# Kernel tuning notes

Measured on AMD Instinct MI355X. Metric: run time of the kernel, lower is better.

Reference implementation:

```python
import jax, jax.numpy as jnp
import numpy as np

ATTN_RNN_DIM, EMB_DIM, ATTN_DIM = 1024, 512, 128
N_FILT, KSIZE = 32, 31
B, T = 64, 2048


def setup_inputs() -> dict:
    key = jax.random.key(0)
    ks = jax.random.split(key, 8)
    return {
        "attention_rnn_h": jax.random.normal(ks[0], (B, ATTN_RNN_DIM), jnp.float32),
        "memory": jax.random.normal(ks[1], (B, T, EMB_DIM), jnp.float32),
        "processed_memory": jax.random.normal(ks[2], (B, T, ATTN_DIM), jnp.float32),
        "attention_weights_cat": jax.random.uniform(ks[3], (B, 2, T), jnp.float32),
        "memory_mask": jnp.zeros((B, T), jnp.bool_),
        # learned params
        "W_query": jax.random.normal(ks[4], (ATTN_DIM, ATTN_RNN_DIM), jnp.float32) * 0.02,
        "conv_w": jax.random.normal(ks[5], (N_FILT, 2, KSIZE), jnp.float32) * 0.05,
        "W_dense": jax.random.normal(ks[6], (ATTN_DIM, N_FILT), jnp.float32) * 0.05,
        "w_v": jax.random.normal(ks[7], (1, ATTN_DIM), jnp.float32) * 0.05,
    }


def reference(attention_rnn_h, memory, processed_memory, attention_weights_cat,
              memory_mask, W_query, conv_w, W_dense, w_v):
    pad = (KSIZE - 1) // 2
    # location conv: (B,2,T) -> (B,N_FILT,T), no bias, 'same' padding
    loc = jax.lax.conv_general_dilated(
        attention_weights_cat, conv_w, window_strides=(1,),
        padding=[(pad, pad)], dimension_numbers=("NCH", "OIH", "NCH"))
    # location dense: (B,T,N_FILT) @ W_dense.T -> (B,T,ATTN_DIM)
    processed_loc = jnp.einsum("bft,df->btd", loc, W_dense)
    # processed query: (B,1,ATTN_DIM)
    processed_query = (attention_rnn_h @ W_query.T)[:, None, :]
    # additive energy: w^T tanh(q + loc + mem) -> (B,T)
    energy = jnp.tanh(processed_query + processed_loc + processed_memory)
    alignment = jnp.einsum("btd,d->bt", energy, w_v[0])
    alignment = jnp.where(memory_mask, -jnp.inf, alignment)
    attention_weights = jax.nn.softmax(alignment, axis=1)  # over T
    # context: (B,1,T) @ (B,T,E) -> (B,E)
    attention_context = jnp.einsum("bt,bte->be", attention_weights, memory)
    return attention_context, attention_weights
```

## Files before the change

kernel.cpp:

```cpp
#include <hip/hip_runtime.h>
#include <math.h>

#define B_SZ 64
#define T_SZ 2048
#define EMB 512
#define ADIM 128
#define NFILT 32
#define KSZ 31
#define TT 64

__device__ __forceinline__ float fast_tanh(float x) {
    float e = __expf(2.f * x);
    return 1.f - 2.f / (e + 1.f);
}

__global__ __launch_bounds__(128) void pq_kernel(const float* __restrict__ h,
                                                 const float* __restrict__ Wq,
                                                 float* __restrict__ pq) {
    const int b = blockIdx.x;
    const int d = threadIdx.x;
    __shared__ float hs[1024];
    for (int i = threadIdx.x; i < 1024; i += 128) hs[i] = h[b * 1024 + i];
    __syncthreads();
    const float4* wr = (const float4*)(Wq + (size_t)d * 1024);
    const float4* hr = (const float4*)hs;
    float acc = 0.f;
    #pragma unroll 8
    for (int k = 0; k < 256; ++k) {
        float4 w = wr[k], x = hr[k];
        acc += w.x * x.x + w.y * x.y + w.z * x.z + w.w * x.w;
    }
    pq[b * 128 + d] = acc;
}

__global__ __launch_bounds__(256) void align_kernel(
    const float* __restrict__ aw_cat,
    const float* __restrict__ pmem,
    const float* __restrict__ pq,
    const float* __restrict__ conv_w,
    const float* __restrict__ W_dense,
    const float* __restrict__ w_v,
    const unsigned char* __restrict__ mask,
    float* __restrict__ align_out)
{
    const int b  = blockIdx.y;
    const int t0 = blockIdx.x * TT;
    const int tid = threadIdx.x;
    const int dq = tid & 31;
    const int tg = tid >> 5;

    __shared__ float cw[NFILT * 62];
    __shared__ float wdT[NFILT * 132];
    __shared__ float aw_s[2][TT + 40];
    __shared__ float locT[NFILT][TT + 8];

    for (int i = tid; i < NFILT * 62; i += 256) cw[i] = conv_w[i];
    for (int i = tid; i < 4096; i += 256) {
        int d = i >> 5, f = i & 31;
        wdT[f * 132 + d] = W_dense[i];
    }
    for (int i = tid; i < 2 * (TT + 40); i += 256) {
        int c = i / (TT + 40), x = i % (TT + 40);
        int t = t0 + x - 15;
        float v = 0.f;
        if (x < TT + 30 && t >= 0 && t < T_SZ)
            v = aw_cat[((size_t)b * 2 + c) * T_SZ + t];
        aw_s[c][x] = v;
    }
    __syncthreads();

    {
        float awr[2][40];
        #pragma unroll
        for (int c = 0; c < 2; ++c)
            #pragma unroll
            for (int q = 0; q < 10; ++q)
                *(float4*)&awr[c][q * 4] = *(const float4*)&aw_s[c][tg * 8 + q * 4];
        float cwr[62];
        #pragma unroll
        for (int q = 0; q < 31; ++q)
            *(float2*)&cwr[q * 2] = *(const float2*)&cw[dq * 62 + q * 2];
        float lres[8];
        #pragma unroll
        for (int j = 0; j < 8; ++j) {
            float acc = 0.f;
            #pragma unroll
            for (int k = 0; k < KSZ; ++k) {
                acc += awr[0][j + k] * cwr[k];
                acc += awr[1][j + k] * cwr[31 + k];
            }
            lres[j] = acc;
        }
        *(float4*)&locT[dq][tg * 8 + 0] = *(float4*)&lres[0];
        *(float4*)&locT[dq][tg * 8 + 4] = *(float4*)&lres[4];
    }
    __syncthreads();

    const float4 pq4 = *(const float4*)&pq[b * 128 + dq * 4];
    const float4 wv4 = *(const float4*)&w_v[dq * 4];

    float4 pm[2][4];
    const float4* pm4 = (const float4*)pmem;
    #pragma unroll
    for (int g = 0; g < 2; ++g)
        #pragma unroll
        for (int jj = 0; jj < 4; ++jj) {
            int tl = tg * 8 + g * 4 + jj;
            pm[g][jj] = pm4[((size_t)(b * T_SZ + t0 + tl)) * 32 + dq];
        }

    float4 acc[2][4];
    #pragma unroll
    for (int g = 0; g < 2; ++g)
        #pragma unroll
        for (int jj = 0; jj < 4; ++jj) acc[g][jj] = make_float4(0.f, 0.f, 0.f, 0.f);

    #pragma unroll
    for (int h = 0; h < 2; ++h) {
        float4 wreg[16];
        #pragma unroll
        for (int f16 = 0; f16 < 16; ++f16)
            wreg[f16] = *(const float4*)&wdT[(h * 16 + f16) * 132 + dq * 4];
        #pragma unroll
        for (int g = 0; g < 2; ++g) {
            #pragma unroll
            for (int f16 = 0; f16 < 16; ++f16) {
                int f = h * 16 + f16;
                float4 lf = *(const float4*)&locT[f][tg * 8 + g * 4];
                float4 w = wreg[f16];
                acc[g][0].x += lf.x * w.x; acc[g][0].y += lf.x * w.y; acc[g][0].z += lf.x * w.z; acc[g][0].w += lf.x * w.w;
                acc[g][1].x += lf.y * w.x; acc[g][1].y += lf.y * w.y; acc[g][1].z += lf.y * w.z; acc[g][1].w += lf.y * w.w;
                acc[g][2].x += lf.z * w.x; acc[g][2].y += lf.z * w.y; acc[g][2].z += lf.z * w.z; acc[g][2].w += lf.z * w.w;
                acc[g][3].x += lf.w * w.x; acc[g][3].y += lf.w * w.y; acc[g][3].z += lf.w * w.z; acc[g][3].w += lf.w * w.w;
            }
        }
    }

    #pragma unroll
    for (int g = 0; g < 2; ++g) {
        #pragma unroll
        for (int jj = 0; jj < 4; ++jj) {
            int tl = tg * 8 + g * 4 + jj;
            float4 a = acc[g][jj];
            float4 p = pm[g][jj];
            float ex = fast_tanh(pq4.x + a.x + p.x);
            float ey = fast_tanh(pq4.y + a.y + p.y);
            float ez = fast_tanh(pq4.z + a.z + p.z);
            float ew = fast_tanh(pq4.w + a.w + p.w);
            float part = ex * wv4.x + ey * wv4.y + ez * wv4.z + ew * wv4.w;
            #pragma unroll
            for (int off = 16; off; off >>= 1) part += __shfl_xor(part, off);
            if (dq == 0) {
                int t = t0 + tl;
                float av = part;
                if (mask[(size_t)b * T_SZ + t]) av = -INFINITY;
                align_out[(size_t)b * T_SZ + t] = av;
            }
        }
    }
}

__global__ __launch_bounds__(256) void softmax_kernel(float* __restrict__ a) {
    const int b = blockIdx.x;
    float* row = a + (size_t)b * T_SZ;
    const int tid = threadIdx.x;
    float v[8];
    #pragma unroll
    for (int i = 0; i < 8; ++i) v[i] = row[tid + 256 * i];
    float m = v[0];
    #pragma unroll
    for (int i = 1; i < 8; ++i) m = fmaxf(m, v[i]);
    #pragma unroll
    for (int off = 32; off; off >>= 1) m = fmaxf(m, __shfl_xor(m, off));
    __shared__ float sm[4];
    __shared__ float ss[4];
    const int wid = tid >> 6;
    if ((tid & 63) == 0) sm[wid] = m;
    __syncthreads();
    m = fmaxf(fmaxf(sm[0], sm[1]), fmaxf(sm[2], sm[3]));
    float e[8], s = 0.f;
    #pragma unroll
    for (int i = 0; i < 8; ++i) { e[i] = __expf(v[i] - m); s += e[i]; }
    #pragma unroll
    for (int off = 32; off; off >>= 1) s += __shfl_xor(s, off);
    if ((tid & 63) == 0) ss[wid] = s;
    __syncthreads();
    float inv = 1.f / (ss[0] + ss[1] + ss[2] + ss[3]);
    #pragma unroll
    for (int i = 0; i < 8; ++i) row[tid + 256 * i] = e[i] * inv;
}

__global__ __launch_bounds__(256) void ctx_kernel(const float* __restrict__ mem,
                                                  const float* __restrict__ w,
                                                  float* __restrict__ out) {
    const int b = blockIdx.y;
    const int chunk = blockIdx.x;
    const int e4 = threadIdx.x & 127;
    const int tt = threadIdx.x >> 7;
    const float4* m4 = (const float4*)(mem + (size_t)b * T_SZ * EMB);
    const float* wr = w + (size_t)b * T_SZ;
    float4 acc = make_float4(0.f, 0.f, 0.f, 0.f);
    const int tb = chunk * 64;
    for (int j = tt; j < 64; j += 2) {
        const int t = tb + j;
        const float wt = wr[t];
        const float4 mm = m4[(size_t)t * 128 + e4];
        acc.x += wt * mm.x; acc.y += wt * mm.y; acc.z += wt * mm.z; acc.w += wt * mm.w;
    }
    __shared__ float4 red[128];
    if (tt) red[e4] = acc;
    __syncthreads();
    if (!tt) {
        const float4 o = red[e4];
        float* dst = out + (size_t)b * EMB + e4 * 4;
        atomicAdd(dst + 0, acc.x + o.x);
        atomicAdd(dst + 1, acc.y + o.y);
        atomicAdd(dst + 2, acc.z + o.z);
        atomicAdd(dst + 3, acc.w + o.w);
    }
}

extern "C" void kernel_launch(void* const* d_in, const int* in_sizes, int n_in,
                              void* d_out, int out_size, void* d_ws, size_t ws_size,
                              hipStream_t stream) {
    const float* h     = (const float*)d_in[0];
    const float* mem   = (const float*)d_in[1];
    const float* pmem  = (const float*)d_in[2];
    const float* awc   = (const float*)d_in[3];
    const unsigned char* mask = (const unsigned char*)d_in[4];
    const float* Wq    = (const float*)d_in[5];
    const float* cw    = (const float*)d_in[6];
    const float* Wd    = (const float*)d_in[7];
    const float* wv    = (const float*)d_in[8];

    float* out = (float*)d_out;
    float* ctx = out;
    float* wts = out + B_SZ * EMB;
    float* pq  = (float*)d_ws;

    hipMemsetAsync(ctx, 0, (size_t)B_SZ * EMB * sizeof(float), stream);
    pq_kernel<<<B_SZ, 128, 0, stream>>>(h, Wq, pq);
    align_kernel<<<dim3(T_SZ / TT, B_SZ), 256, 0, stream>>>(awc, pmem, pq, cw, Wd, wv, mask, wts);
    softmax_kernel<<<B_SZ, 256, 0, stream>>>(wts);
    ctx_kernel<<<dim3(T_SZ / 64, B_SZ), 256, 0, stream>>>(mem, wts, ctx);
}
```

Baseline: 520.0 us.

## Parallelize query projection, fold ctx zeroing, restructure conv, nontemporal ctx loads

```diff
diff --git a/kernel.cpp b/kernel.cpp
--- a/kernel.cpp
+++ b/kernel.cpp
@@ -9,28 +9,33 @@
 #define KSZ 31
 #define TT 64
 
+typedef float f4v __attribute__((ext_vector_type(4)));
+
 __device__ __forceinline__ float fast_tanh(float x) {
     float e = __expf(2.f * x);
     return 1.f - 2.f / (e + 1.f);
 }
 
-__global__ __launch_bounds__(128) void pq_kernel(const float* __restrict__ h,
+__global__ __launch_bounds__(256) void pq_kernel(const float* __restrict__ h,
                                                  const float* __restrict__ Wq,
-                                                 float* __restrict__ pq) {
-    const int b = blockIdx.x;
-    const int d = threadIdx.x;
-    __shared__ float hs[1024];
-    for (int i = threadIdx.x; i < 1024; i += 128) hs[i] = h[b * 1024 + i];
-    __syncthreads();
+                                                 float* __restrict__ pq,
+                                                 float* __restrict__ ctx) {
+    const int b = blockIdx.y, dg = blockIdx.x;
+    const int w = threadIdx.x >> 6, lane = threadIdx.x & 63;
+    if (threadIdx.x < 16) ctx[b * EMB + dg * 16 + threadIdx.x] = 0.f;
+    const int d = dg * 4 + w;
     const float4* wr = (const float4*)(Wq + (size_t)d * 1024);
-    const float4* hr = (const float4*)hs;
+    const float4* hr = (const float4*)(h + (size_t)b * 1024);
     float acc = 0.f;
-    #pragma unroll 8
-    for (int k = 0; k < 256; ++k) {
-        float4 w = wr[k], x = hr[k];
-        acc += w.x * x.x + w.y * x.y + w.z * x.z + w.w * x.w;
-    }
-    pq[b * 128 + d] = acc;
+    #pragma unroll
+    for (int it = 0; it < 4; ++it) {
+        float4 a = wr[lane + 64 * it];
+        float4 x = hr[lane + 64 * it];
+        acc += a.x * x.x + a.y * x.y + a.z * x.z + a.w * x.w;
+    }
+    #pragma unroll
+    for (int off = 32; off; off >>= 1) acc += __shfl_xor(acc, off);
+    if (lane == 0) pq[b * 128 + d] = acc;
 }
 
 __global__ __launch_bounds__(256) void align_kernel(
@@ -76,20 +81,18 @@
             #pragma unroll
             for (int q = 0; q < 10; ++q)
                 *(float4*)&awr[c][q * 4] = *(const float4*)&aw_s[c][tg * 8 + q * 4];
-        float cwr[62];
-        #pragma unroll
-        for (int q = 0; q < 31; ++q)
-            *(float2*)&cwr[q * 2] = *(const float2*)&cw[dq * 62 + q * 2];
         float lres[8];
         #pragma unroll
-        for (int j = 0; j < 8; ++j) {
-            float acc = 0.f;
-            #pragma unroll
-            for (int k = 0; k < KSZ; ++k) {
-                acc += awr[0][j + k] * cwr[k];
-                acc += awr[1][j + k] * cwr[31 + k];
+        for (int j = 0; j < 8; ++j) lres[j] = 0.f;
+        #pragma unroll
+        for (int k = 0; k < KSZ; ++k) {
+            float c0 = cw[dq * 62 + k];
+            float c1 = cw[dq * 62 + 31 + k];
+            #pragma unroll
+            for (int j = 0; j < 8; ++j) {
+                lres[j] += awr[0][j + k] * c0;
+                lres[j] += awr[1][j + k] * c1;
             }
-            lres[j] = acc;
         }
         *(float4*)&locT[dq][tg * 8 + 0] = *(float4*)&lres[0];
         *(float4*)&locT[dq][tg * 8 + 4] = *(float4*)&lres[4];
@@ -197,21 +200,26 @@
     const int chunk = blockIdx.x;
     const int e4 = threadIdx.x & 127;
     const int tt = threadIdx.x >> 7;
-    const float4* m4 = (const float4*)(mem + (size_t)b * T_SZ * EMB);
-    const float* wr = w + (size_t)b * T_SZ;
-    float4 acc = make_float4(0.f, 0.f, 0.f, 0.f);
     const int tb = chunk * 64;
+
+    __shared__ float ws_[64];
+    if (threadIdx.x < 64) ws_[threadIdx.x] = w[(size_t)b * T_SZ + tb + threadIdx.x];
+    __syncthreads();
+
+    const f4v* m4 = (const f4v*)(mem + (size_t)b * T_SZ * EMB) + (size_t)tb * 128 + e4;
+    f4v acc = (f4v){0.f, 0.f, 0.f, 0.f};
+    #pragma unroll 8
     for (int j = tt; j < 64; j += 2) {
-        const int t = tb + j;
-        const float wt = wr[t];
-        const float4 mm = m4[(size_t)t * 128 + e4];
-        acc.x += wt * mm.x; acc.y += wt * mm.y; acc.z += wt * mm.z; acc.w += wt * mm.w;
-    }
-    __shared__ float4 red[128];
+        f4v mm = __builtin_nontemporal_load(&m4[(size_t)j * 128]);
+        float wt = ws_[j];
+        acc += wt * mm;
+    }
+
+    __shared__ f4v red[128];
     if (tt) red[e4] = acc;
     __syncthreads();
     if (!tt) {
-        const float4 o = red[e4];
+        f4v o = red[e4];
         float* dst = out + (size_t)b * EMB + e4 * 4;
         atomicAdd(dst + 0, acc.x + o.x);
         atomicAdd(dst + 1, acc.y + o.y);
@@ -238,8 +246,7 @@
     float* wts = out + B_SZ * EMB;
     float* pq  = (float*)d_ws;
 
-    hipMemsetAsync(ctx, 0, (size_t)B_SZ * EMB * sizeof(float), stream);
-    pq_kernel<<<B_SZ, 128, 0, stream>>>(h, Wq, pq);
+    pq_kernel<<<dim3(32, B_SZ), 256, 0, stream>>>(h, Wq, pq, ctx);
     align_kernel<<<dim3(T_SZ / TT, B_SZ), 256, 0, stream>>>(awc, pmem, pq, cw, Wd, wv, mask, wts);
     softmax_kernel<<<B_SZ, 256, 0, stream>>>(wts);
     ctx_kernel<<<dim3(T_SZ / 64, B_SZ), 256, 0, stream>>>(mem, wts, ctx);
```

Result: faster. 469.6 us (-9.7%).
